# Kernel optimization log

Hardware: AMD Instinct MI355X
Metric: run time of the kernel (lower is better)

The kernel has to match this reference:

```python
import jax, jax.numpy as jnp
import numpy as np
from jax import lax

BN_EPS = 1e-5
SQ_EPS = 1e-8


def squash(s, axis=-1):
    # v = (|s|^2 / (1+|s|^2)) * s / |s|
    n2 = jnp.sum(s * s, axis=axis, keepdims=True)
    return (n2 / (1.0 + n2)) * s / jnp.sqrt(n2 + SQ_EPS)


def setup_inputs() -> dict:
    key = jax.random.key(0)
    ks = jax.random.split(key, 5)
    B, C, H, W = 64, 512, 28, 28
    NUM_ROUTES = 8 * 10 * 10  # lower_num_caps * 10 * 10 after k9 s2 conv on 28x28
    features = jax.random.normal(ks[0], (B, C, H, W), jnp.float32)
    conv1_w = jax.random.normal(ks[1], (256, 512, 3, 3), jnp.float32) * 0.02
    conv1_b = jnp.zeros((256,), jnp.float32)
    bn_gamma = jnp.ones((256,), jnp.float32)
    bn_beta = jnp.zeros((256,), jnp.float32)
    bn_mean = jnp.zeros((256,), jnp.float32)
    bn_var = jnp.ones((256,), jnp.float32)
    prim_w = jax.random.normal(ks[2], (256, 256, 9, 9), jnp.float32) * 0.02
    prim_b = jnp.zeros((256,), jnp.float32)
    # routing transform: (num_routes, higher_num_caps, out_dim, in_dim)
    route_w = jax.random.normal(ks[3], (NUM_ROUTES, 2, 16, 32), jnp.float32) * 0.05
    return {"features": features, "conv1_w": conv1_w, "conv1_b": conv1_b,
            "bn_gamma": bn_gamma, "bn_beta": bn_beta, "bn_mean": bn_mean,
            "bn_var": bn_var, "prim_w": prim_w, "prim_b": prim_b,
            "route_w": route_w}


def reference(features, conv1_w, conv1_b, bn_gamma, bn_beta, bn_mean, bn_var,
              prim_w, prim_b, route_w):
    B = features.shape[0]
    dn = ("NCHW", "OIHW", "NCHW")
    # pre_conv: Conv2d(512->256, k3, pad1) + BatchNorm (eval) + ReLU
    x = lax.conv_general_dilated(features, conv1_w, (1, 1), "SAME",
                                 dimension_numbers=dn)
    x = x + conv1_b[None, :, None, None]
    inv = bn_gamma * lax.rsqrt(bn_var + BN_EPS)
    x = x * inv[None, :, None, None] + (bn_beta - bn_mean * inv)[None, :, None, None]
    x = jax.nn.relu(x)
    # primary capsules: Conv2d(256->8*32, k9, s2, valid) -> (B,256,10,10)
    p = lax.conv_general_dilated(x, prim_w, (2, 2), "VALID",
                                 dimension_numbers=dn)
    p = p + prim_b[None, :, None, None]
    Hp, Wp = p.shape[2], p.shape[3]
    # (B, num_caps, cap_dim, Hp*Wp) -> (B, num_caps*Hp*Wp, cap_dim)
    p = p.reshape(B, 8, 32, Hp * Wp).transpose(0, 1, 3, 2).reshape(B, 8 * Hp * Wp, 32)
    lower_caps = squash(p, axis=-1)  # (B, 800, 32)
    # predictions u_hat: (B, routes, higher_caps, out_dim)
    u_hat = jnp.einsum("bri,rjoi->brjo", lower_caps, route_w)
    # dynamic routing-by-agreement
    b = jnp.zeros((B, u_hat.shape[1], u_hat.shape[2]), u_hat.dtype)
    n_iter = 3
    for it in range(n_iter):
        c = jax.nn.softmax(b, axis=2)                  # coupling coeffs
        s = jnp.einsum("brj,brjo->bjo", c, u_hat)      # weighted sum
        v = squash(s, axis=-1)                          # (B, 2, 16)
        if it < n_iter - 1:
            b = b + jnp.einsum("brjo,bjo->brj", u_hat, v)
    return (lower_caps, v)
```

## Files before the change

kernel.cpp:

```cpp
#include <hip/hip_runtime.h>
#include <hip/hip_bf16.h>

#define BN_EPS 1e-5f
#define SQ_EPS 1e-8f

typedef __hip_bfloat16 bf16;
typedef __attribute__((ext_vector_type(8))) short bf16x8;
typedef __attribute__((ext_vector_type(4))) float f32x4;

__device__ __forceinline__ void gload_lds16(const void* g, void* l) {
    __builtin_amdgcn_global_load_lds(
        (const __attribute__((address_space(1))) unsigned int*)g,
        (__attribute__((address_space(3))) unsigned int*)l, 16, 0, 0);
}

__device__ __forceinline__ unsigned short f2bfu(float f) {
    bf16 h = __float2bfloat16(f);
    return *(unsigned short*)&h;
}

__global__ __launch_bounds__(256) void feat_to_nhwc(
    const float* __restrict__ feat, bf16* __restrict__ featP) {
    int b = blockIdx.z, ct = blockIdx.y, pt = blockIdx.x;
    int ci0 = ct * 64, px0 = pt * 64;
    int tid = threadIdx.x;
    __shared__ float t[64][65];
#pragma unroll
    for (int rep = 0; rep < 16; rep++) {
        int ci_l = rep * 4 + (tid >> 6);
        int px = px0 + (tid & 63);
        float v = 0.f;
        if (px < 784) v = feat[(b * 512 + ci0 + ci_l) * 784 + px];
        t[ci_l][tid & 63] = v;
    }
    __syncthreads();
#pragma unroll
    for (int rep = 0; rep < 4; rep++) {
        int px_l = rep * 16 + (tid >> 4);
        int px = px0 + px_l;
        if (px < 784) {
            int h = px / 28, wq = px % 28;
            int ci = (tid & 15) * 4;
            ushort4 o;
            o.x = f2bfu(t[ci + 0][px_l]);
            o.y = f2bfu(t[ci + 1][px_l]);
            o.z = f2bfu(t[ci + 2][px_l]);
            o.w = f2bfu(t[ci + 3][px_l]);
            *(ushort4*)&featP[((b * 30 + h + 1) * 30 + (wq + 1)) * 512 + ci0 + ci] = o;
        }
    }
}

__global__ __launch_bounds__(256) void zero_ring(bf16* __restrict__ featP) {
    int b = blockIdx.x;
    uint4 zz = {0u, 0u, 0u, 0u};
    for (int i = threadIdx.x; i < 116 * 64; i += 256) {
        int rp = i >> 6;
        int ci = (i & 63) * 8;
        int hp, wp;
        if (rp < 30)      { hp = 0;       wp = rp; }
        else if (rp < 60) { hp = 29;      wp = rp - 30; }
        else if (rp < 88) { hp = rp - 59; wp = 0; }
        else              { hp = rp - 87; wp = 29; }
        *(uint4*)&featP[(b * 900 + hp * 30 + wp) * 512 + ci] = zz;
    }
}

__global__ __launch_bounds__(256) void wF_transform(
    const float* __restrict__ w1, const float* __restrict__ w2,
    bf16* __restrict__ wt1F, bf16* __restrict__ wt2F) {
    __shared__ float tt[10368];
    if (blockIdx.x < 256) {
        int co = blockIdx.x;
        const float* src = w1 + co * 4608;
        for (int i = threadIdx.x; i < 4608; i += 256) tt[i] = src[i];
        __syncthreads();
        int co16 = co >> 4, l15 = co & 15;
        for (int i = threadIdx.x; i < 576; i += 256) {
            int g = i >> 6, cc = (i >> 2) & 15, kq = i & 3;
            short v[8];
#pragma unroll
            for (int j = 0; j < 8; j++) {
                unsigned short u = f2bfu(tt[(cc * 32 + kq * 8 + j) * 9 + g]);
                v[j] = (short)u;
            }
            int fidx = cc * 9 + g;
            bf16x8* dst = (bf16x8*)&wt1F[(fidx * 16 + co16) * 512 + (kq * 16 + l15) * 8];
            bf16x8 pk = {v[0], v[1], v[2], v[3], v[4], v[5], v[6], v[7]};
            *dst = pk;
        }
    } else {
        int bid = blockIdx.x - 256;
        int half = bid & 1, co = bid >> 1;
        const float* src = w2 + co * 20736 + half * 10368;
        for (int i = threadIdx.x; i < 10368; i += 256) tt[i] = src[i];
        __syncthreads();
        int co16 = co >> 4, l15 = co & 15;
        for (int i = threadIdx.x; i < 1296; i += 256) {
            int sh = i >> 4, ccl = (i >> 2) & 3, kq = i & 3;
            int z = sh / 10; if (z > 7) z = 7;
            int s0 = (81 * z) >> 3;
            int ns = ((81 * (z + 1)) >> 3) - s0;
            int fidx = s0 * 8 + (half * 4 + ccl) * ns + (sh - s0);
            short v[8];
#pragma unroll
            for (int j = 0; j < 8; j++) {
                unsigned short u = f2bfu(tt[(ccl * 32 + kq * 8 + j) * 81 + sh]);
                v[j] = (short)u;
            }
            bf16x8* dst = (bf16x8*)&wt2F[(fidx * 16 + co16) * 512 + (kq * 16 + l15) * 8];
            bf16x8 pk = {v[0], v[1], v[2], v[3], v[4], v[5], v[6], v[7]};
            *dst = pk;
        }
    }
}

__global__ __launch_bounds__(512, 4) void conv1_mfma(
    const bf16* __restrict__ featP, const bf16* __restrict__ wt1F,
    const float* __restrict__ bias, const float* __restrict__ gamma,
    const float* __restrict__ beta, const float* __restrict__ mean,
    const float* __restrict__ var, bf16* __restrict__ x) {
    __shared__ char As4[4 * 7168];
    const int tid = threadIdx.x, lane = tid & 63, w = tid >> 6;
    const int Mt = blockIdx.x;

    const bf16* pA0;
    {
        int r0 = (w << 4) + (lane >> 2);
        int q = (lane & 3) ^ ((r0 >> 1) & 3);
        int m0 = Mt * 112 + (w < 7 ? r0 : 0);
        int b0 = m0 / 784, rr = m0 % 784, h0 = rr / 28, w0 = rr % 28;
        pA0 = featP + ((b0 * 30 + h0) * 30 + w0) * 512 + q * 8;
    }
    const bf16x8* pB = (const bf16x8*)wt1F + w * 128 + lane;

    int a_off[7];
#pragma unroll
    for (int mi = 0; mi < 7; mi++) {
        int r = mi * 16 + (lane & 15);
        a_off[mi] = r * 64 + (((lane >> 4) ^ ((r >> 1) & 3)) * 16);
    }

    f32x4 acc[7][2];
#pragma unroll
    for (int i = 0; i < 7; i++)
#pragma unroll
        for (int j = 0; j < 2; j++) acc[i][j] = f32x4{0.f, 0.f, 0.f, 0.f};

    bf16x8 Bv0[2], Bv1[2];

#define STG1(bi, offE)                                                     \
    do {                                                                   \
        if (w < 7)                                                         \
            gload_lds16(pA0 + (offE), As4 + (bi) * 7168 + w * 1024);       \
    } while (0)

    STG1(0, 0); STG1(1, 512); STG1(2, 1024);
    { const bf16x8* bp = pB; Bv0[0] = bp[0]; Bv0[1] = bp[64]; }
    asm volatile("s_waitcnt vmcnt(2)" ::: "memory");
    __builtin_amdgcn_s_barrier();
    asm volatile("" ::: "memory");

#define C1_STEP(u, BU, BL)                                                 \
    do {                                                                   \
        const int t_ = t + (u);                                            \
        int ttc = t_ + 3; if (ttc > 143) ttc = 143;                        \
        {       \
            int cc_ = ttc / 9, g_ = ttc - 9 * cc_;                         \
            int ky_ = g_ / 3, kx_ = g_ - 3 * ky_;                          \
            STG1((u + 3) & 3, (ky_ * 30 + kx_) * 512 + cc_ * 32);          \
        }                                                                  \
        {                                                                  \
            int fn = t_ + 1; if (fn > 143) fn = 143;                       \
            const bf16x8* bp = pB + fn * 1024;                             \
            BL[0] = bp[0]; BL[1] = bp[64];                                 \
        }                                                                  \
        const char* Ab = As4 + (u) * 7168;                                 \
        bf16x8 af[7];                                                      \
        _Pragma("unroll")                                                  \
        for (int mi = 0; mi < 7; mi++)                                     \
            af[mi] = *(const bf16x8*)(Ab + a_off[mi]);                     \
        __builtin_amdgcn_s_setprio(1);                                     \
        _Pragma("unroll")                                                  \
        for (int nj = 0; nj < 2; nj++)                                     \
            _Pragma("unroll")                                              \
            for (int mi = 0; mi < 7; mi++)                                 \
                acc[mi][nj] = __builtin_amdgcn_mfma_f32_16x16x32_bf16(     \
                    af[mi], BU[nj], acc[mi][nj], 0, 0, 0);                 \
        __builtin_amdgcn_s_setprio(0);                                     \
        if (t_ < 143) {                                                    \
            asm volatile("s_waitcnt vmcnt(8)" ::: "memory");               \
            __builtin_amdgcn_s_barrier();                                  \
            asm volatile("" ::: "memory");                                 \
        }                                                                  \
    } while (0)

    for (int t = 0; t < 144; t += 4) {
        C1_STEP(0, Bv0, Bv1);
        C1_STEP(1, Bv1, Bv0);
        C1_STEP(2, Bv0, Bv1);
        C1_STEP(3, Bv1, Bv0);
    }

#pragma unroll
    for (int nj = 0; nj < 2; nj++) {
        int co = w * 32 + nj * 16 + (lane & 15);
        float inv = gamma[co] * rsqrtf(var[co] + BN_EPS);
        float sh = beta[co] - mean[co] * inv;
        float bs = bias[co];
#pragma unroll
        for (int mi = 0; mi < 7; mi++) {
            int m0 = Mt * 112 + mi * 16 + ((lane >> 4) << 2);
#pragma unroll
            for (int r = 0; r < 4; r++) {
                float v = (acc[mi][nj][r] + bs) * inv + sh;
                x[(m0 + r) * 256 + co] = __float2bfloat16(fmaxf(v, 0.f));
            }
        }
    }
#undef STG1
#undef C1_STEP
}

__global__ __launch_bounds__(256, 2) void conv2_mfma(
    const bf16* __restrict__ x, const bf16* __restrict__ wt2F,
    bf16* __restrict__ p_parts) {
    __shared__ char As4[4 * 8192];
    const int tid = threadIdx.x, lane = tid & 63, w = tid >> 6;
    const int z = blockIdx.x & 7, Mt = blockIdx.x >> 3;
    const int sh0 = (81 * z) >> 3, sh1 = (81 * (z + 1)) >> 3;
    const int nsh = sh1 - sh0;
    const int NT = nsh << 3;
    const int FB = sh0 << 3;

    const bf16 *pA0, *pA1;
    {
        int r0 = (w << 5) + (lane >> 2);
        int q0 = (lane & 3) ^ ((r0 >> 1) & 3);
        int m0 = Mt * 128 + r0;
        int b0 = m0 / 100, s0 = m0 % 100, ho0 = s0 / 10, wo0 = s0 % 10;
        pA0 = x + ((b0 * 28 + 2 * ho0) * 28 + 2 * wo0) * 256 + q0 * 8;
        int r1 = r0 + 16;
        int q1 = (lane & 3) ^ ((r1 >> 1) & 3);
        int m1 = Mt * 128 + r1;
        int b1 = m1 / 100, s1 = m1 % 100, ho1 = s1 / 10, wo1 = s1 % 10;
        pA1 = x + ((b1 * 28 + 2 * ho1) * 28 + 2 * wo1) * 256 + q1 * 8;
    }
    const bf16x8* pB = (const bf16x8*)wt2F + w * 256 + lane;

    int a_off[8];
#pragma unroll
    for (int mi = 0; mi < 8; mi++) {
        int r = mi * 16 + (lane & 15);
        a_off[mi] = r * 64 + (((lane >> 4) ^ ((r >> 1) & 3)) * 16);
    }

    f32x4 acc[8][4];
#pragma unroll
    for (int i = 0; i < 8; i++)
#pragma unroll
        for (int j = 0; j < 4; j++) acc[i][j] = f32x4{0.f, 0.f, 0.f, 0.f};

    bf16x8 Bv0[4], Bv1[4];

#define STG2(bi, offE)                                                     \
    do {                                                                   \
        gload_lds16(pA0 + (offE), As4 + (bi) * 8192 + w * 2048);           \
        gload_lds16(pA1 + (offE), As4 + (bi) * 8192 + w * 2048 + 1024);    \
    } while (0)

#define A2OFF(tt)                                                          \
    ({ int ttc_ = (tt) < NT ? (tt) : NT - 1;                               \
       int cc_ = ttc_ / nsh, si_ = ttc_ - cc_ * nsh;                       \
       int sh_ = sh0 + si_;                                                \
       int ky_ = sh_ / 9, kx_ = sh_ - 9 * ky_;                             \
       (ky_ * 28 + kx_) * 256 + cc_ * 32; })

    STG2(0, A2OFF(0)); STG2(1, A2OFF(1)); STG2(2, A2OFF(2));
    { const bf16x8* bp = pB + FB * 1024;
      Bv0[0] = bp[0]; Bv0[1] = bp[64]; Bv0[2] = bp[128]; Bv0[3] = bp[192]; }
    asm volatile("s_waitcnt vmcnt(8)" ::: "memory");
    __builtin_amdgcn_s_barrier();
    asm volatile("" ::: "memory");

#define C2_STEP(u, BU, BL)                                                 \
    do {                                                                   \
        const int t_ = t + (u);                                            \
        STG2((u + 3) & 3, A2OFF(t_ + 3));                                  \
        {                                                                  \
            int fn = t_ + 1; if (fn > NT - 1) fn = NT - 1;                 \
            const bf16x8* bp = pB + (FB + fn) * 1024;                      \
            BL[0] = bp[0]; BL[1] = bp[64];                                 \
            BL[2] = bp[128]; BL[3] = bp[192];                              \
        }                                                                  \
        const char* Ab = As4 + (u) * 8192;                                 \
        bf16x8 af[8];                                                      \
        _Pragma("unroll")                                                  \
        for (int mi = 0; mi < 8; mi++)                                     \
            af[mi] = *(const bf16x8*)(Ab + a_off[mi]);                     \
        __builtin_amdgcn_s_setprio(1);                                     \
        _Pragma("unroll")                                                  \
        for (int nj = 0; nj < 4; nj++)                                     \
            _Pragma("unroll")                                              \
            for (int mi = 0; mi < 8; mi++)                                 \
                acc[mi][nj] = __builtin_amdgcn_mfma_f32_16x16x32_bf16(     \
                    af[mi], BU[nj], acc[mi][nj], 0, 0, 0);                 \
        __builtin_amdgcn_s_setprio(0);                                     \
        if (t_ < NT - 1) {                                                 \
            asm volatile("s_waitcnt vmcnt(16)" ::: "memory");              \
            __builtin_amdgcn_s_barrier();                                  \
            asm volatile("" ::: "memory");                                 \
        }                                                                  \
    } while (0)

    for (int t = 0; t < NT; t += 4) {
        C2_STEP(0, Bv0, Bv1);
        C2_STEP(1, Bv1, Bv0);
        C2_STEP(2, Bv0, Bv1);
        C2_STEP(3, Bv1, Bv0);
    }

#pragma unroll
    for (int nj = 0; nj < 4; nj++) {
        int co = w * 64 + nj * 16 + (lane & 15);
#pragma unroll
        for (int mi = 0; mi < 8; mi++) {
            int m0 = Mt * 128 + mi * 16 + ((lane >> 4) << 2);
#pragma unroll
            for (int r = 0; r < 4; r++)
                p_parts[(z * 6400 + m0 + r) * 256 + co] =
                    __float2bfloat16(acc[mi][nj][r]);
        }
    }
#undef STG2
#undef A2OFF
#undef C2_STEP
}

__global__ __launch_bounds__(256) void squash_kernel(
    const bf16* __restrict__ pp, const float* __restrict__ pb,
    float* __restrict__ lc) {
    int rowg = blockIdx.x * 8 + (threadIdx.x >> 5);
    int i = threadIdx.x & 31;
    int b = rowg / 800, r = rowg - b * 800;
    int cap = r / 100, s = r - cap * 100;
    int m = b * 100 + s, co = cap * 32 + i;
    float val = pb[co];
#pragma unroll
    for (int zz = 0; zz < 8; zz++)
        val += __bfloat162float(pp[(zz * 6400 + m) * 256 + co]);
    float n2 = val * val;
#pragma unroll
    for (int msk = 1; msk < 32; msk <<= 1) n2 += __shfl_xor(n2, msk);
    float scale = n2 / ((1.f + n2) * sqrtf(n2 + SQ_EPS));
    lc[(b * 800 + r) * 32 + i] = val * scale;
}

__global__ __launch_bounds__(256) void uhat_kernel(
    const float* __restrict__ lc, const float* __restrict__ rw,
    bf16* __restrict__ uht) {
    int rT = blockIdx.x, bT = blockIdx.y;
    int rl = threadIdx.x >> 5, jo = threadIdx.x & 31;
    int r = rT * 8 + rl;
    float4 wreg[8];
    const float4* wp4 = reinterpret_cast<const float4*>(rw + (r * 32 + jo) * 32);
#pragma unroll
    for (int k = 0; k < 8; k++) wreg[k] = wp4[k];
    for (int b = bT * 16; b < bT * 16 + 16; b++) {
        const float4* lp4 = reinterpret_cast<const float4*>(lc + (b * 800 + r) * 32);
        float acc = 0.f;
#pragma unroll
        for (int k = 0; k < 8; k++) {
            float4 a = lp4[k];
            acc = fmaf(a.x, wreg[k].x, acc);
            acc = fmaf(a.y, wreg[k].y, acc);
            acc = fmaf(a.z, wreg[k].z, acc);
            acc = fmaf(a.w, wreg[k].w, acc);
        }
        uht[(b * 32 + jo) * 800 + r] = __float2bfloat16(acc);
    }
}

__global__ __launch_bounds__(256) void route_all(
    const bf16* __restrict__ uht, float* __restrict__ vout) {
    extern __shared__ float rs[];
    float* u = rs;
    float* lg = rs + 26400;
    float* red = lg + 1600;
    float* vs = red + 256;
    int b = blockIdx.x, tid = threadIdx.x;
    for (int i = tid; i < 25600; i += 256) {
        int jo = i / 800, r = i - jo * 800;
        u[r * 33 + jo] = __bfloat162float(uht[(b * 32 + jo) * 800 + r]);
    }
    for (int i = tid; i < 1600; i += 256) lg[i] = 0.f;
    __syncthreads();
    int jo = tid & 31, rg = tid >> 5;
    for (int it = 0; it < 3; it++) {
        float sp = 0.f;
        for (int r = rg; r < 800; r += 8) {
            float l0 = lg[r * 2], l1 = lg[r * 2 + 1];
            float m = fmaxf(l0, l1);
            float e0 = __expf(l0 - m), e1 = __expf(l1 - m);
            float c = ((jo < 16) ? e0 : e1) / (e0 + e1);
            sp += c * u[r * 33 + jo];
        }
        red[rg * 32 + jo] = sp;
        __syncthreads();
        if (tid < 32) {
            float s = 0.f;
#pragma unroll
            for (int k = 0; k < 8; k++) s += red[k * 32 + tid];
            float n2 = s * s;
#pragma unroll
            for (int m = 1; m < 16; m <<= 1) n2 += __shfl_xor(n2, m);
            float scale = n2 / ((1.f + n2) * sqrtf(n2 + SQ_EPS));
            float v = s * scale;
            vs[tid] = v;
            if (it == 2) vout[b * 32 + tid] = v;
        }
        __syncthreads();
        if (it < 2) {
            for (int r = tid; r < 800; r += 256) {
                float d0 = 0.f, d1 = 0.f;
#pragma unroll
                for (int o = 0; o < 16; o++) {
                    d0 += u[r * 33 + o] * vs[o];
                    d1 += u[r * 33 + 16 + o] * vs[16 + o];
                }
                lg[r * 2] += d0;
                lg[r * 2 + 1] += d1;
            }
            __syncthreads();
        }
    }
}

extern "C" void kernel_launch(void* const* d_in, const int* in_sizes, int n_in,
                              void* d_out, int out_size, void* d_ws, size_t ws_size,
                              hipStream_t stream) {
    const float* feat    = (const float*)d_in[0];
    const float* conv1_w = (const float*)d_in[1];
    const float* conv1_b = (const float*)d_in[2];
    const float* bn_g    = (const float*)d_in[3];
    const float* bn_b    = (const float*)d_in[4];
    const float* bn_m    = (const float*)d_in[5];
    const float* bn_v    = (const float*)d_in[6];
    const float* prim_w  = (const float*)d_in[7];
    const float* prim_b  = (const float*)d_in[8];
    const float* route_w = (const float*)d_in[9];
    float* out = (float*)d_out;

    char* wsb = (char*)d_ws;
    bf16*  featP   = (bf16*)(wsb + 0);
    bf16*  p_parts = (bf16*)(wsb + 0);
    bf16*  uht     = (bf16*)(wsb + 26214400);
    bf16*  x       = (bf16*)(wsb + 58982400);
    bf16*  wt1F    = (bf16*)(wsb + 84672512);
    bf16*  wt2F    = (bf16*)(wsb + 87031808);

    float* lc_out = out;
    float* v_out  = out + 64 * 800 * 32;

    hipFuncSetAttribute((const void*)route_all,
                        hipFuncAttributeMaxDynamicSharedMemorySize, 113152);

    feat_to_nhwc<<<dim3(13, 8, 64), 256, 0, stream>>>(feat, featP);
    zero_ring<<<64, 256, 0, stream>>>(featP);
    wF_transform<<<768, 256, 0, stream>>>(conv1_w, prim_w, wt1F, wt2F);

    conv1_mfma<<<448, 512, 0, stream>>>(
        featP, wt1F, conv1_b, bn_g, bn_b, bn_m, bn_v, x);

    conv2_mfma<<<400, 256, 0, stream>>>(x, wt2F, p_parts);

    squash_kernel<<<6400, 256, 0, stream>>>(p_parts, prim_b, lc_out);

    uhat_kernel<<<dim3(100, 4), 256, 0, stream>>>(lc_out, route_w, uht);

    route_all<<<64, 256, 113152, stream>>>(uht, v_out);
}
```

Baseline: 307.0 us.

## Retile conv kernels to 128x256 blocks with 2x4 wave grid

Both implicit-GEMM conv kernels now use 512-thread blocks arranged as a 2x4 wave grid. Each wave computes a 64x64 output sub-tile (4x4 MFMA accumulators) instead of tall thin strips. Conv1 moves from 112-row tiles with an idle staging wave to 128-row tiles across 392 blocks, and its blocks are remapped so consecutive M-tiles share an XCD. This balances A and B fragment reuse per wave and cuts register use in conv2 so more waves fit. In exchange, B weight loads per wave double in conv1, and the prologue waits for all loads to finish.

```diff
diff --git a/kernel.cpp b/kernel.cpp
--- a/kernel.cpp
+++ b/kernel.cpp
@@ -120,44 +120,44 @@
     const float* __restrict__ bias, const float* __restrict__ gamma,
     const float* __restrict__ beta, const float* __restrict__ mean,
     const float* __restrict__ var, bf16* __restrict__ x) {
-    __shared__ char As4[4 * 7168];
+    __shared__ char As4[4 * 8192];
     const int tid = threadIdx.x, lane = tid & 63, w = tid >> 6;
-    const int Mt = blockIdx.x;
+    const int wr = w >> 2, wc = w & 3;
+    const int xcd = blockIdx.x & 7, ix = blockIdx.x >> 3;
+    const int Mt = xcd * 49 + ix;
 
     const bf16* pA0;
     {
         int r0 = (w << 4) + (lane >> 2);
         int q = (lane & 3) ^ ((r0 >> 1) & 3);
-        int m0 = Mt * 112 + (w < 7 ? r0 : 0);
+        int m0 = Mt * 128 + r0;
         int b0 = m0 / 784, rr = m0 % 784, h0 = rr / 28, w0 = rr % 28;
         pA0 = featP + ((b0 * 30 + h0) * 30 + w0) * 512 + q * 8;
     }
-    const bf16x8* pB = (const bf16x8*)wt1F + w * 128 + lane;
-
-    int a_off[7];
-#pragma unroll
-    for (int mi = 0; mi < 7; mi++) {
-        int r = mi * 16 + (lane & 15);
+    const bf16x8* pB = (const bf16x8*)wt1F + wc * 256 + lane;
+
+    int a_off[4];
+#pragma unroll
+    for (int mi = 0; mi < 4; mi++) {
+        int r = wr * 64 + mi * 16 + (lane & 15);
         a_off[mi] = r * 64 + (((lane >> 4) ^ ((r >> 1) & 3)) * 16);
     }
 
-    f32x4 acc[7][2];
-#pragma unroll
-    for (int i = 0; i < 7; i++)
-#pragma unroll
-        for (int j = 0; j < 2; j++) acc[i][j] = f32x4{0.f, 0.f, 0.f, 0.f};
-
-    bf16x8 Bv0[2], Bv1[2];
+    f32x4 acc[4][4];
+#pragma unroll
+    for (int i = 0; i < 4; i++)
+#pragma unroll
+        for (int j = 0; j < 4; j++) acc[i][j] = f32x4{0.f, 0.f, 0.f, 0.f};
+
+    bf16x8 Bv0[4], Bv1[4];
 
 #define STG1(bi, offE)                                                     \
-    do {                                                                   \
-        if (w < 7)                                                         \
-            gload_lds16(pA0 + (offE), As4 + (bi) * 7168 + w * 1024);       \
-    } while (0)
+    gload_lds16(pA0 + (offE), As4 + (bi) * 8192 + w * 1024)
 
     STG1(0, 0); STG1(1, 512); STG1(2, 1024);
-    { const bf16x8* bp = pB; Bv0[0] = bp[0]; Bv0[1] = bp[64]; }
-    asm volatile("s_waitcnt vmcnt(2)" ::: "memory");
+    { const bf16x8* bp = pB;
+      Bv0[0] = bp[0]; Bv0[1] = bp[64]; Bv0[2] = bp[128]; Bv0[3] = bp[192]; }
+    asm volatile("s_waitcnt vmcnt(0)" ::: "memory");
     __builtin_amdgcn_s_barrier();
     asm volatile("" ::: "memory");
 
@@ -174,22 +174,23 @@
             int fn = t_ + 1; if (fn > 143) fn = 143;                       \
             const bf16x8* bp = pB + fn * 1024;                             \
             BL[0] = bp[0]; BL[1] = bp[64];                                 \
+            BL[2] = bp[128]; BL[3] = bp[192];                              \
         }                                                                  \
-        const char* Ab = As4 + (u) * 7168;                                 \
-        bf16x8 af[7];                                                      \
+        const char* Ab = As4 + (u) * 8192;                                 \
+        bf16x8 af[4];                                                      \
         _Pragma("unroll")                                                  \
-        for (int mi = 0; mi < 7; mi++)                                     \
+        for (int mi = 0; mi < 4; mi++)                                     \
             af[mi] = *(const bf16x8*)(Ab + a_off[mi]);                     \
         __builtin_amdgcn_s_setprio(1);                                     \
         _Pragma("unroll")                                                  \
-        for (int nj = 0; nj < 2; nj++)                                     \
+        for (int nj = 0; nj < 4; nj++)                                     \
             _Pragma("unroll")                                              \
-            for (int mi = 0; mi < 7; mi++)                                 \
+            for (int mi = 0; mi < 4; mi++)                                 \
                 acc[mi][nj] = __builtin_amdgcn_mfma_f32_16x16x32_bf16(     \
                     af[mi], BU[nj], acc[mi][nj], 0, 0, 0);                 \
         __builtin_amdgcn_s_setprio(0);                                     \
         if (t_ < 143) {                                                    \
-            asm volatile("s_waitcnt vmcnt(8)" ::: "memory");               \
+            asm volatile("s_waitcnt vmcnt(10)" ::: "memory");              \
             __builtin_amdgcn_s_barrier();                                  \
             asm volatile("" ::: "memory");                                 \
         }                                                                  \
@@ -203,14 +204,14 @@
     }
 
 #pragma unroll
-    for (int nj = 0; nj < 2; nj++) {
-        int co = w * 32 + nj * 16 + (lane & 15);
+    for (int nj = 0; nj < 4; nj++) {
+        int co = wc * 64 + nj * 16 + (lane & 15);
         float inv = gamma[co] * rsqrtf(var[co] + BN_EPS);
         float sh = beta[co] - mean[co] * inv;
         float bs = bias[co];
 #pragma unroll
-        for (int mi = 0; mi < 7; mi++) {
-            int m0 = Mt * 112 + mi * 16 + ((lane >> 4) << 2);
+        for (int mi = 0; mi < 4; mi++) {
+            int m0 = Mt * 128 + wr * 64 + mi * 16 + ((lane >> 4) << 2);
 #pragma unroll
             for (int r = 0; r < 4; r++) {
                 float v = (acc[mi][nj][r] + bs) * inv + sh;
@@ -222,52 +223,45 @@
 #undef C1_STEP
 }
 
-__global__ __launch_bounds__(256, 2) void conv2_mfma(
+__global__ __launch_bounds__(512, 4) void conv2_mfma(
     const bf16* __restrict__ x, const bf16* __restrict__ wt2F,
     bf16* __restrict__ p_parts) {
     __shared__ char As4[4 * 8192];
     const int tid = threadIdx.x, lane = tid & 63, w = tid >> 6;
+    const int wr = w >> 2, wc = w & 3;
     const int z = blockIdx.x & 7, Mt = blockIdx.x >> 3;
     const int sh0 = (81 * z) >> 3, sh1 = (81 * (z + 1)) >> 3;
     const int nsh = sh1 - sh0;
     const int NT = nsh << 3;
     const int FB = sh0 << 3;
 
-    const bf16 *pA0, *pA1;
+    const bf16* pA0;
     {
-        int r0 = (w << 5) + (lane >> 2);
-        int q0 = (lane & 3) ^ ((r0 >> 1) & 3);
+        int r0 = (w << 4) + (lane >> 2);
+        int q = (lane & 3) ^ ((r0 >> 1) & 3);
         int m0 = Mt * 128 + r0;
         int b0 = m0 / 100, s0 = m0 % 100, ho0 = s0 / 10, wo0 = s0 % 10;
-        pA0 = x + ((b0 * 28 + 2 * ho0) * 28 + 2 * wo0) * 256 + q0 * 8;
-        int r1 = r0 + 16;
-        int q1 = (lane & 3) ^ ((r1 >> 1) & 3);
-        int m1 = Mt * 128 + r1;
-        int b1 = m1 / 100, s1 = m1 % 100, ho1 = s1 / 10, wo1 = s1 % 10;
-        pA1 = x + ((b1 * 28 + 2 * ho1) * 28 + 2 * wo1) * 256 + q1 * 8;
-    }
-    const bf16x8* pB = (const bf16x8*)wt2F + w * 256 + lane;
-
-    int a_off[8];
-#pragma unroll
-    for (int mi = 0; mi < 8; mi++) {
-        int r = mi * 16 + (lane & 15);
+        pA0 = x + ((b0 * 28 + 2 * ho0) * 28 + 2 * wo0) * 256 + q * 8;
+    }
+    const bf16x8* pB = (const bf16x8*)wt2F + wc * 256 + lane;
+
+    int a_off[4];
+#pragma unroll
+    for (int mi = 0; mi < 4; mi++) {
+        int r = wr * 64 + mi * 16 + (lane & 15);
         a_off[mi] = r * 64 + (((lane >> 4) ^ ((r >> 1) & 3)) * 16);
     }
 
-    f32x4 acc[8][4];
-#pragma unroll
-    for (int i = 0; i < 8; i++)
+    f32x4 acc[4][4];
+#pragma unroll
+    for (int i = 0; i < 4; i++)
 #pragma unroll
         for (int j = 0; j < 4; j++) acc[i][j] = f32x4{0.f, 0.f, 0.f, 0.f};
 
     bf16x8 Bv0[4], Bv1[4];
 
 #define STG2(bi, offE)                                                     \
-    do {                                                                   \
-        gload_lds16(pA0 + (offE), As4 + (bi) * 8192 + w * 2048);           \
-        gload_lds16(pA1 + (offE), As4 + (bi) * 8192 + w * 2048 + 1024);    \
-    } while (0)
+    gload_lds16(pA0 + (offE), As4 + (bi) * 8192 + w * 1024)
 
 #define A2OFF(tt)                                                          \
     ({ int ttc_ = (tt) < NT ? (tt) : NT - 1;                               \
@@ -279,7 +273,7 @@
     STG2(0, A2OFF(0)); STG2(1, A2OFF(1)); STG2(2, A2OFF(2));
     { const bf16x8* bp = pB + FB * 1024;
       Bv0[0] = bp[0]; Bv0[1] = bp[64]; Bv0[2] = bp[128]; Bv0[3] = bp[192]; }
-    asm volatile("s_waitcnt vmcnt(8)" ::: "memory");
+    asm volatile("s_waitcnt vmcnt(0)" ::: "memory");
     __builtin_amdgcn_s_barrier();
     asm volatile("" ::: "memory");
 
@@ -294,20 +288,20 @@
             BL[2] = bp[128]; BL[3] = bp[192];                              \
         }                                                                  \
         const char* Ab = As4 + (u) * 8192;                                 \
-        bf16x8 af[8];                                                      \
+        bf16x8 af[4];                                                      \
         _Pragma("unroll")                                                  \
-        for (int mi = 0; mi < 8; mi++)                                     \
+        for (int mi = 0; mi < 4; mi++)                                     \
             af[mi] = *(const bf16x8*)(Ab + a_off[mi]);                     \
         __builtin_amdgcn_s_setprio(1);                                     \
         _Pragma("unroll")                                                  \
         for (int nj = 0; nj < 4; nj++)                                     \
             _Pragma("unroll")                                              \
-            for (int mi = 0; mi < 8; mi++)                                 \
+            for (int mi = 0; mi < 4; mi++)                                 \
                 acc[mi][nj] = __builtin_amdgcn_mfma_f32_16x16x32_bf16(     \
                     af[mi], BU[nj], acc[mi][nj], 0, 0, 0);                 \
         __builtin_amdgcn_s_setprio(0);                                     \
         if (t_ < NT - 1) {                                                 \
-            asm volatile("s_waitcnt vmcnt(16)" ::: "memory");              \
+            asm volatile("s_waitcnt vmcnt(10)" ::: "memory");              \
             __builtin_amdgcn_s_barrier();                                  \
             asm volatile("" ::: "memory");                                 \
         }                                                                  \
@@ -322,10 +316,10 @@
 
 #pragma unroll
     for (int nj = 0; nj < 4; nj++) {
-        int co = w * 64 + nj * 16 + (lane & 15);
-#pragma unroll
-        for (int mi = 0; mi < 8; mi++) {
-            int m0 = Mt * 128 + mi * 16 + ((lane >> 4) << 2);
+        int co = wc * 64 + nj * 16 + (lane & 15);
+#pragma unroll
+        for (int mi = 0; mi < 4; mi++) {
+            int m0 = Mt * 128 + wr * 64 + mi * 16 + ((lane >> 4) << 2);
 #pragma unroll
             for (int r = 0; r < 4; r++)
                 p_parts[(z * 6400 + m0 + r) * 256 + co] =
@@ -469,10 +463,10 @@
     zero_ring<<<64, 256, 0, stream>>>(featP);
     wF_transform<<<768, 256, 0, stream>>>(conv1_w, prim_w, wt1F, wt2F);
 
-    conv1_mfma<<<448, 512, 0, stream>>>(
+    conv1_mfma<<<392, 512, 0, stream>>>(
         featP, wt1F, conv1_b, bn_g, bn_b, bn_m, bn_v, x);
 
-    conv2_mfma<<<400, 256, 0, stream>>>(x, wt2F, p_parts);
+    conv2_mfma<<<400, 512, 0, stream>>>(x, wt2F, p_parts);
 
     squash_kernel<<<6400, 256, 0, stream>>>(p_parts, prim_b, lc_out);
 
```

Measured after the change: 345.5 us. 1.13x slower.

## Fuse squash into u_hat kernel, fold ring zeroing into weight transform, tighten waits

Applied to the files above, without the earlier changes.

The padding-ring zeroing moves into extra blocks of the weight-transform kernel, which removes one launch. The squash and u_hat kernels become a single 100-block kernel that loops over all 64 batches. Each squashed row is staged through shared memory and consumed at once, so the lower-capsule tensor is no longer reread from global memory. The vmcnt waits in both conv mainloops become stricter, which shortens how far loads run ahead of compute and may hurt overlap in the dominant conv kernels. The fused kernel also has much lower parallelism, with each block processing the batches serially.

```diff
diff --git a/kernel.cpp b/kernel.cpp
--- a/kernel.cpp
+++ b/kernel.cpp
@@ -51,25 +51,26 @@
     }
 }
 
-__global__ __launch_bounds__(256) void zero_ring(bf16* __restrict__ featP) {
-    int b = blockIdx.x;
-    uint4 zz = {0u, 0u, 0u, 0u};
-    for (int i = threadIdx.x; i < 116 * 64; i += 256) {
-        int rp = i >> 6;
-        int ci = (i & 63) * 8;
-        int hp, wp;
-        if (rp < 30)      { hp = 0;       wp = rp; }
-        else if (rp < 60) { hp = 29;      wp = rp - 30; }
-        else if (rp < 88) { hp = rp - 59; wp = 0; }
-        else              { hp = rp - 87; wp = 29; }
-        *(uint4*)&featP[(b * 900 + hp * 30 + wp) * 512 + ci] = zz;
-    }
-}
-
 __global__ __launch_bounds__(256) void wF_transform(
     const float* __restrict__ w1, const float* __restrict__ w2,
-    bf16* __restrict__ wt1F, bf16* __restrict__ wt2F) {
+    bf16* __restrict__ wt1F, bf16* __restrict__ wt2F,
+    bf16* __restrict__ featP) {
     __shared__ float tt[10368];
+    if (blockIdx.x >= 768) {
+        int b = blockIdx.x - 768;
+        uint4 zz = {0u, 0u, 0u, 0u};
+        for (int i = threadIdx.x; i < 116 * 64; i += 256) {
+            int rp = i >> 6;
+            int ci = (i & 63) * 8;
+            int hp, wp;
+            if (rp < 30)      { hp = 0;       wp = rp; }
+            else if (rp < 60) { hp = 29;      wp = rp - 30; }
+            else if (rp < 88) { hp = rp - 59; wp = 0; }
+            else              { hp = rp - 87; wp = 29; }
+            *(uint4*)&featP[(b * 900 + hp * 30 + wp) * 512 + ci] = zz;
+        }
+        return;
+    }
     if (blockIdx.x < 256) {
         int co = blockIdx.x;
         const float* src = w1 + co * 4608;
@@ -189,7 +190,7 @@
                     af[mi], BU[nj], acc[mi][nj], 0, 0, 0);                 \
         __builtin_amdgcn_s_setprio(0);                                     \
         if (t_ < 143) {                                                    \
-            asm volatile("s_waitcnt vmcnt(8)" ::: "memory");               \
+            asm volatile("s_waitcnt vmcnt(2)" ::: "memory");               \
             __builtin_amdgcn_s_barrier();                                  \
             asm volatile("" ::: "memory");                                 \
         }                                                                  \
@@ -279,7 +280,7 @@
     STG2(0, A2OFF(0)); STG2(1, A2OFF(1)); STG2(2, A2OFF(2));
     { const bf16x8* bp = pB + FB * 1024;
       Bv0[0] = bp[0]; Bv0[1] = bp[64]; Bv0[2] = bp[128]; Bv0[3] = bp[192]; }
-    asm volatile("s_waitcnt vmcnt(8)" ::: "memory");
+    asm volatile("s_waitcnt vmcnt(4)" ::: "memory");
     __builtin_amdgcn_s_barrier();
     asm volatile("" ::: "memory");
 
@@ -307,7 +308,7 @@
                     af[mi], BU[nj], acc[mi][nj], 0, 0, 0);                 \
         __builtin_amdgcn_s_setprio(0);                                     \
         if (t_ < NT - 1) {                                                 \
-            asm volatile("s_waitcnt vmcnt(16)" ::: "memory");              \
+            asm volatile("s_waitcnt vmcnt(4)" ::: "memory");               \
             __builtin_amdgcn_s_barrier();                                  \
             asm volatile("" ::: "memory");                                 \
         }                                                                  \
@@ -337,41 +338,38 @@
 #undef C2_STEP
 }
 
-__global__ __launch_bounds__(256) void squash_kernel(
+__global__ __launch_bounds__(256) void squash_uhat(
     const bf16* __restrict__ pp, const float* __restrict__ pb,
-    float* __restrict__ lc) {
-    int rowg = blockIdx.x * 8 + (threadIdx.x >> 5);
-    int i = threadIdx.x & 31;
-    int b = rowg / 800, r = rowg - b * 800;
-    int cap = r / 100, s = r - cap * 100;
-    int m = b * 100 + s, co = cap * 32 + i;
-    float val = pb[co];
-#pragma unroll
-    for (int zz = 0; zz < 8; zz++)
-        val += __bfloat162float(pp[(zz * 6400 + m) * 256 + co]);
-    float n2 = val * val;
-#pragma unroll
-    for (int msk = 1; msk < 32; msk <<= 1) n2 += __shfl_xor(n2, msk);
-    float scale = n2 / ((1.f + n2) * sqrtf(n2 + SQ_EPS));
-    lc[(b * 800 + r) * 32 + i] = val * scale;
-}
-
-__global__ __launch_bounds__(256) void uhat_kernel(
-    const float* __restrict__ lc, const float* __restrict__ rw,
+    const float* __restrict__ rw, float* __restrict__ lc,
     bf16* __restrict__ uht) {
-    int rT = blockIdx.x, bT = blockIdx.y;
+    int rT = blockIdx.x;
     int rl = threadIdx.x >> 5, jo = threadIdx.x & 31;
     int r = rT * 8 + rl;
     float4 wreg[8];
-    const float4* wp4 = reinterpret_cast<const float4*>(rw + (r * 32 + jo) * 32);
+    const float4* wp4 = (const float4*)(rw + (r * 32 + jo) * 32);
 #pragma unroll
     for (int k = 0; k < 8; k++) wreg[k] = wp4[k];
-    for (int b = bT * 16; b < bT * 16 + 16; b++) {
-        const float4* lp4 = reinterpret_cast<const float4*>(lc + (b * 800 + r) * 32);
+    int cap = r / 100, s = r - cap * 100;
+    int co = cap * 32 + jo;
+    float bsv = pb[co];
+    __shared__ float vrow[8][32];
+    for (int b = 0; b < 64; b++) {
+        int m = b * 100 + s;
+        float val = bsv;
+#pragma unroll
+        for (int z = 0; z < 8; z++)
+            val += __bfloat162float(pp[(z * 6400 + m) * 256 + co]);
+        float n2 = val * val;
+#pragma unroll
+        for (int msk = 1; msk < 32; msk <<= 1) n2 += __shfl_xor(n2, msk);
+        float scale = n2 / ((1.f + n2) * sqrtf(n2 + SQ_EPS));
+        float sval = val * scale;
+        lc[(b * 800 + r) * 32 + jo] = sval;
+        vrow[rl][jo] = sval;
         float acc = 0.f;
 #pragma unroll
         for (int k = 0; k < 8; k++) {
-            float4 a = lp4[k];
+            float4 a = *(const float4*)&vrow[rl][k * 4];
             acc = fmaf(a.x, wreg[k].x, acc);
             acc = fmaf(a.y, wreg[k].y, acc);
             acc = fmaf(a.z, wreg[k].z, acc);
@@ -466,17 +464,14 @@
                         hipFuncAttributeMaxDynamicSharedMemorySize, 113152);
 
     feat_to_nhwc<<<dim3(13, 8, 64), 256, 0, stream>>>(feat, featP);
-    zero_ring<<<64, 256, 0, stream>>>(featP);
-    wF_transform<<<768, 256, 0, stream>>>(conv1_w, prim_w, wt1F, wt2F);
+    wF_transform<<<832, 256, 0, stream>>>(conv1_w, prim_w, wt1F, wt2F, featP);
 
     conv1_mfma<<<448, 512, 0, stream>>>(
         featP, wt1F, conv1_b, bn_g, bn_b, bn_m, bn_v, x);
 
     conv2_mfma<<<400, 256, 0, stream>>>(x, wt2F, p_parts);
 
-    squash_kernel<<<6400, 256, 0, stream>>>(p_parts, prim_b, lc_out);
-
-    uhat_kernel<<<dim3(100, 4), 256, 0, stream>>>(lc_out, route_w, uht);
+    squash_uhat<<<100, 256, 0, stream>>>(p_parts, prim_b, route_w, lc_out, uht);
 
     route_all<<<64, 256, 113152, stream>>>(uht, v_out);
 }
```

Result: slower. 342.9 us (+11.7%).

## Split conv2 work across 8 waves and fold ring zeroing into weight transform

Applied to the files above, without the earlier changes.

The conv2 kernel now launches 512 threads per block instead of 256. Each wave stages one A row-group and computes 32 output channels instead of 64, which halves the per-wave accumulator and B-fragment registers and allows more waves per CU for latency hiding. The zero_ring kernel is merged into wF_transform as extra blocks, which removes one kernel launch. In exchange, A-tile LDS reads are duplicated across more waves and 8 waves now take part in each barrier, which could raise sync overhead.

```diff
diff --git a/kernel.cpp b/kernel.cpp
--- a/kernel.cpp
+++ b/kernel.cpp
@@ -51,25 +51,26 @@
     }
 }
 
-__global__ __launch_bounds__(256) void zero_ring(bf16* __restrict__ featP) {
-    int b = blockIdx.x;
-    uint4 zz = {0u, 0u, 0u, 0u};
-    for (int i = threadIdx.x; i < 116 * 64; i += 256) {
-        int rp = i >> 6;
-        int ci = (i & 63) * 8;
-        int hp, wp;
-        if (rp < 30)      { hp = 0;       wp = rp; }
-        else if (rp < 60) { hp = 29;      wp = rp - 30; }
-        else if (rp < 88) { hp = rp - 59; wp = 0; }
-        else              { hp = rp - 87; wp = 29; }
-        *(uint4*)&featP[(b * 900 + hp * 30 + wp) * 512 + ci] = zz;
-    }
-}
-
 __global__ __launch_bounds__(256) void wF_transform(
     const float* __restrict__ w1, const float* __restrict__ w2,
-    bf16* __restrict__ wt1F, bf16* __restrict__ wt2F) {
+    bf16* __restrict__ wt1F, bf16* __restrict__ wt2F,
+    bf16* __restrict__ featP) {
     __shared__ float tt[10368];
+    if (blockIdx.x >= 768) {
+        int b = blockIdx.x - 768;
+        uint4 zz = {0u, 0u, 0u, 0u};
+        for (int i = threadIdx.x; i < 116 * 64; i += 256) {
+            int rp = i >> 6;
+            int ci = (i & 63) * 8;
+            int hp, wp;
+            if (rp < 30)      { hp = 0;       wp = rp; }
+            else if (rp < 60) { hp = 29;      wp = rp - 30; }
+            else if (rp < 88) { hp = rp - 59; wp = 0; }
+            else              { hp = rp - 87; wp = 29; }
+            *(uint4*)&featP[(b * 900 + hp * 30 + wp) * 512 + ci] = zz;
+        }
+        return;
+    }
     if (blockIdx.x < 256) {
         int co = blockIdx.x;
         const float* src = w1 + co * 4608;
@@ -222,7 +223,7 @@
 #undef C1_STEP
 }
 
-__global__ __launch_bounds__(256, 2) void conv2_mfma(
+__global__ __launch_bounds__(512, 4) void conv2_mfma(
     const bf16* __restrict__ x, const bf16* __restrict__ wt2F,
     bf16* __restrict__ p_parts) {
     __shared__ char As4[4 * 8192];
@@ -233,20 +234,15 @@
     const int NT = nsh << 3;
     const int FB = sh0 << 3;
 
-    const bf16 *pA0, *pA1;
+    const bf16* pA0;
     {
-        int r0 = (w << 5) + (lane >> 2);
-        int q0 = (lane & 3) ^ ((r0 >> 1) & 3);
+        int r0 = (w << 4) + (lane >> 2);
+        int q = (lane & 3) ^ ((r0 >> 1) & 3);
         int m0 = Mt * 128 + r0;
         int b0 = m0 / 100, s0 = m0 % 100, ho0 = s0 / 10, wo0 = s0 % 10;
-        pA0 = x + ((b0 * 28 + 2 * ho0) * 28 + 2 * wo0) * 256 + q0 * 8;
-        int r1 = r0 + 16;
-        int q1 = (lane & 3) ^ ((r1 >> 1) & 3);
-        int m1 = Mt * 128 + r1;
-        int b1 = m1 / 100, s1 = m1 % 100, ho1 = s1 / 10, wo1 = s1 % 10;
-        pA1 = x + ((b1 * 28 + 2 * ho1) * 28 + 2 * wo1) * 256 + q1 * 8;
-    }
-    const bf16x8* pB = (const bf16x8*)wt2F + w * 256 + lane;
+        pA0 = x + ((b0 * 28 + 2 * ho0) * 28 + 2 * wo0) * 256 + q * 8;
+    }
+    const bf16x8* pB = (const bf16x8*)wt2F + w * 128 + lane;
 
     int a_off[8];
 #pragma unroll
@@ -255,19 +251,16 @@
         a_off[mi] = r * 64 + (((lane >> 4) ^ ((r >> 1) & 3)) * 16);
     }
 
-    f32x4 acc[8][4];
+    f32x4 acc[8][2];
 #pragma unroll
     for (int i = 0; i < 8; i++)
 #pragma unroll
-        for (int j = 0; j < 4; j++) acc[i][j] = f32x4{0.f, 0.f, 0.f, 0.f};
-
-    bf16x8 Bv0[4], Bv1[4];
+        for (int j = 0; j < 2; j++) acc[i][j] = f32x4{0.f, 0.f, 0.f, 0.f};
+
+    bf16x8 Bv0[2], Bv1[2];
 
 #define STG2(bi, offE)                                                     \
-    do {                                                                   \
-        gload_lds16(pA0 + (offE), As4 + (bi) * 8192 + w * 2048);           \
-        gload_lds16(pA1 + (offE), As4 + (bi) * 8192 + w * 2048 + 1024);    \
-    } while (0)
+    gload_lds16(pA0 + (offE), As4 + (bi) * 8192 + w * 1024)
 
 #define A2OFF(tt)                                                          \
     ({ int ttc_ = (tt) < NT ? (tt) : NT - 1;                               \
@@ -277,9 +270,8 @@
        (ky_ * 28 + kx_) * 256 + cc_ * 32; })
 
     STG2(0, A2OFF(0)); STG2(1, A2OFF(1)); STG2(2, A2OFF(2));
-    { const bf16x8* bp = pB + FB * 1024;
-      Bv0[0] = bp[0]; Bv0[1] = bp[64]; Bv0[2] = bp[128]; Bv0[3] = bp[192]; }
-    asm volatile("s_waitcnt vmcnt(8)" ::: "memory");
+    { const bf16x8* bp = pB + FB * 1024; Bv0[0] = bp[0]; Bv0[1] = bp[64]; }
+    asm volatile("s_waitcnt vmcnt(2)" ::: "memory");
     __builtin_amdgcn_s_barrier();
     asm volatile("" ::: "memory");
 
@@ -291,7 +283,6 @@
             int fn = t_ + 1; if (fn > NT - 1) fn = NT - 1;                 \
             const bf16x8* bp = pB + (FB + fn) * 1024;                      \
             BL[0] = bp[0]; BL[1] = bp[64];                                 \
-            BL[2] = bp[128]; BL[3] = bp[192];                              \
         }                                                                  \
         const char* Ab = As4 + (u) * 8192;                                 \
         bf16x8 af[8];                                                      \
@@ -300,14 +291,14 @@
             af[mi] = *(const bf16x8*)(Ab + a_off[mi]);                     \
         __builtin_amdgcn_s_setprio(1);                                     \
         _Pragma("unroll")                                                  \
-        for (int nj = 0; nj < 4; nj++)                                     \
+        for (int nj = 0; nj < 2; nj++)                                     \
             _Pragma("unroll")                                              \
             for (int mi = 0; mi < 8; mi++)                                 \
                 acc[mi][nj] = __builtin_amdgcn_mfma_f32_16x16x32_bf16(     \
                     af[mi], BU[nj], acc[mi][nj], 0, 0, 0);                 \
         __builtin_amdgcn_s_setprio(0);                                     \
         if (t_ < NT - 1) {                                                 \
-            asm volatile("s_waitcnt vmcnt(16)" ::: "memory");              \
+            asm volatile("s_waitcnt vmcnt(8)" ::: "memory");               \
             __builtin_amdgcn_s_barrier();                                  \
             asm volatile("" ::: "memory");                                 \
         }                                                                  \
@@ -321,8 +312,8 @@
     }
 
 #pragma unroll
-    for (int nj = 0; nj < 4; nj++) {
-        int co = w * 64 + nj * 16 + (lane & 15);
+    for (int nj = 0; nj < 2; nj++) {
+        int co = w * 32 + nj * 16 + (lane & 15);
 #pragma unroll
         for (int mi = 0; mi < 8; mi++) {
             int m0 = Mt * 128 + mi * 16 + ((lane >> 4) << 2);
@@ -466,13 +457,12 @@
                         hipFuncAttributeMaxDynamicSharedMemorySize, 113152);
 
     feat_to_nhwc<<<dim3(13, 8, 64), 256, 0, stream>>>(feat, featP);
-    zero_ring<<<64, 256, 0, stream>>>(featP);
-    wF_transform<<<768, 256, 0, stream>>>(conv1_w, prim_w, wt1F, wt2F);
+    wF_transform<<<832, 256, 0, stream>>>(conv1_w, prim_w, wt1F, wt2F, featP);
 
     conv1_mfma<<<448, 512, 0, stream>>>(
         featP, wt1F, conv1_b, bn_g, bn_b, bn_m, bn_v, x);
 
-    conv2_mfma<<<400, 256, 0, stream>>>(x, wt2F, p_parts);
+    conv2_mfma<<<400, 512, 0, stream>>>(x, wt2F, p_parts);
 
     squash_kernel<<<6400, 256, 0, stream>>>(p_parts, prim_b, lc_out);
 
```

Measured after the change: 300.0 us. 2.3% less time.
